# Kernel optimization log

Hardware: AMD Instinct MI355X
Metric: run time of the kernel (lower is better)

Reference implementation:

```python
import jax, jax.numpy as jnp
import numpy as np

B, T, C = 2, 1024, 512
H, KVH = 8, 4
HD = C // H          # head_dim = 64
D2 = HD // 2         # rotary half = 32
SCALE = 1.0 / np.sqrt(HD)


def setup_inputs() -> dict:
    key = jax.random.key(0)
    ks = jax.random.split(key, 5)
    x = jax.random.normal(ks[0], (B, T, C), jnp.float32)
    # RoPE tables: [1, T, 1, D2] broadcastable over (B, T, H, HD/2)
    inv_freq = 1.0 / (10000.0 ** (jnp.arange(D2, dtype=jnp.float32) / D2))
    ang = jnp.arange(T, dtype=jnp.float32)[:, None] * inv_freq[None, :]
    cos = jnp.cos(ang)[None, :, None, :]
    sin = jnp.sin(ang)[None, :, None, :]
    s = 1.0 / np.sqrt(C)
    Wq = jax.random.normal(ks[1], (C, H * HD), jnp.float32) * s
    Wk = jax.random.normal(ks[2], (C, KVH * HD), jnp.float32) * s
    Wv = jax.random.normal(ks[3], (C, KVH * HD), jnp.float32) * s
    Wo = jax.random.normal(ks[4], (C, C), jnp.float32) * s
    return {"x": x, "cos": cos, "sin": sin, "Wq": Wq, "Wk": Wk, "Wv": Wv, "Wo": Wo}


def _rope(t, cos, sin):
    d = t.shape[-1] // 2
    t1, t2 = t[..., :d], t[..., d:]
    return jnp.concatenate([t1 * cos + t2 * sin, -t1 * sin + t2 * cos], axis=-1)


def reference(x, cos, sin, Wq, Wk, Wv, Wo):
    b, t, c = x.shape
    q = (x @ Wq).reshape(b, t, H, HD)
    k = (x @ Wk).reshape(b, t, KVH, HD)
    v = (x @ Wv).reshape(b, t, KVH, HD)
    q = _rope(q, cos, sin)
    k = _rope(k, cos, sin)
    q = q.transpose(0, 2, 1, 3)                      # [B,H,T,HD]
    k = k.transpose(0, 2, 1, 3)                      # [B,KVH,T,HD]
    v = v.transpose(0, 2, 1, 3)
    n_rep = H // KVH
    k = jnp.repeat(k, n_rep, axis=1)                 # GQA expand -> [B,H,T,HD]
    v = jnp.repeat(v, n_rep, axis=1)
    logits = jnp.einsum('bhqd,bhkd->bhqk', q, k) * SCALE
    mask = jnp.triu(jnp.full((t, t), -jnp.inf, dtype=logits.dtype), 1)
    A = jax.nn.softmax(logits + mask, axis=-1)       # [B,H,T,T]
    A_plus_I = A + jnp.eye(t, dtype=A.dtype)
    y = jnp.linalg.solve(A_plus_I, v)                # batched LU solve, (A+I)^-1 @ V
    y = y.transpose(0, 2, 1, 3).reshape(b, t, c)
    return x + y @ Wo
```

## Files before the change

kernel.cpp:

```cpp
#include <hip/hip_runtime.h>
#include <cmath>

#define TT 1024
#define HH 8
#define KVHN 4

typedef unsigned short u16;
typedef __attribute__((ext_vector_type(8))) short bf16x8;
typedef __attribute__((ext_vector_type(4))) float f32x4;

#define MFMA(a, b, c) __builtin_amdgcn_mfma_f32_16x16x32_bf16(a, b, c, 0, 0, 0)

__device__ __forceinline__ float bflo(unsigned u) { return __uint_as_float(u << 16); }
__device__ __forceinline__ float bfhi(unsigned u) { return __uint_as_float(u & 0xffff0000u); }
__device__ __forceinline__ u16 bfr(float f) {
  unsigned u = __float_as_uint(f);
  return (u16)((u + 0x7fffu + ((u >> 16) & 1u)) >> 16);
}
__device__ __forceinline__ float hpart(u16 h) {
  return __uint_as_float((unsigned)h << 16);
}

__device__ __forceinline__ bf16x8 ld8_g(const u16* __restrict__ p) {
  uint4 v = *reinterpret_cast<const uint4*>(p);
  return __builtin_bit_cast(bf16x8, v);
}
__device__ __forceinline__ bf16x8 ld8_lds(const u16* s, int col, int k8) {
  const uint4* p = reinterpret_cast<const uint4*>(s);
  return __builtin_bit_cast(bf16x8, p[col * 8 + (k8 ^ (col & 7))]);
}
__device__ __forceinline__ void st_split_lds(u16* sh, u16* sl, int col, int r0,
                                             f32x4 v) {
  u16 hh[4], ll[4];
#pragma unroll
  for (int j = 0; j < 4; ++j) {
    u16 hb = bfr(v[j]);
    hh[j] = hb;
    ll[j] = bfr(v[j] - hpart(hb));
  }
  uint2 ph, pl;
  ph.x = (unsigned)hh[0] | ((unsigned)hh[1] << 16);
  ph.y = (unsigned)hh[2] | ((unsigned)hh[3] << 16);
  pl.x = (unsigned)ll[0] | ((unsigned)ll[1] << 16);
  pl.y = (unsigned)ll[2] | ((unsigned)ll[3] << 16);
  int idx = col * 64 + (((r0 >> 3) ^ (col & 7)) << 3) + (r0 & 7);
  *reinterpret_cast<uint2*>(sh + idx) = ph;
  *reinterpret_cast<uint2*>(sl + idx) = pl;
}
__device__ __forceinline__ void cvt8v(float4 a, float4 b, bf16x8& h, bf16x8& l) {
  float v[8] = {a.x, a.y, a.z, a.w, b.x, b.y, b.z, b.w};
  unsigned hh[8], ll[8];
#pragma unroll
  for (int j = 0; j < 8; ++j) {
    u16 hb = bfr(v[j]);
    hh[j] = hb;
    ll[j] = bfr(v[j] - hpart(hb));
  }
  uint4 H, L;
  H.x = hh[0] | (hh[1] << 16); H.y = hh[2] | (hh[3] << 16);
  H.z = hh[4] | (hh[5] << 16); H.w = hh[6] | (hh[7] << 16);
  L.x = ll[0] | (ll[1] << 16); L.y = ll[2] | (ll[3] << 16);
  L.z = ll[4] | (ll[5] << 16); L.w = ll[6] | (ll[7] << 16);
  h = __builtin_bit_cast(bf16x8, H);
  l = __builtin_bit_cast(bf16x8, L);
}
__device__ __forceinline__ void cvt8(const float* __restrict__ p, bf16x8& h,
                                     bf16x8& l) {
  float4 a = *reinterpret_cast<const float4*>(p);
  float4 b = *reinterpret_cast<const float4*>(p + 4);
  cvt8v(a, b, h, l);
}

__global__ __launch_bounds__(256) void prep_kernel(
    const float* __restrict__ x, const float* __restrict__ Wq,
    const float* __restrict__ Wk, const float* __restrict__ Wv,
    const float* __restrict__ Wo, u16* __restrict__ WtH, u16* __restrict__ WtL,
    u16* __restrict__ WotH, u16* __restrict__ WotL, u16* __restrict__ Xh,
    u16* __restrict__ Xl) {
  const int kt = blockIdx.x, nt = blockIdx.y;
  const int tid = threadIdx.x;
  const int k0 = kt * 64;

  if (nt >= 24) {
    const int r0 = (nt - 24) * 64;
    const int rr = tid >> 2, kc0 = (tid & 3) * 16;
    const float* src = x + (size_t)(r0 + rr) * 512 + k0 + kc0;
    u16* dh = Xh + (size_t)(r0 + rr) * 512 + k0 + kc0;
    u16* dl = Xl + (size_t)(r0 + rr) * 512 + k0 + kc0;
#pragma unroll
    for (int m = 0; m < 4; ++m) {
      float4 v = *reinterpret_cast<const float4*>(src + m * 4);
      float vv[4] = {v.x, v.y, v.z, v.w};
      u16 hh[4], ll[4];
#pragma unroll
      for (int j = 0; j < 4; ++j) {
        u16 hb = bfr(vv[j]);
        hh[j] = hb;
        ll[j] = bfr(vv[j] - hpart(hb));
      }
      uint2 ph, pl;
      ph.x = (unsigned)hh[0] | ((unsigned)hh[1] << 16);
      ph.y = (unsigned)hh[2] | ((unsigned)hh[3] << 16);
      pl.x = (unsigned)ll[0] | ((unsigned)ll[1] << 16);
      pl.y = (unsigned)ll[2] | ((unsigned)ll[3] << 16);
      *reinterpret_cast<uint2*>(dh + m * 4) = ph;
      *reinterpret_cast<uint2*>(dl + m * 4) = pl;
    }
    return;
  }

  const float* Wsel;
  int wstride, wc0;
  u16 *oh, *ol;
  if (nt < 16) {
    if (nt < 8) { Wsel = Wq; wstride = 512; wc0 = nt * 64; }
    else if (nt < 12) { Wsel = Wk; wstride = 256; wc0 = (nt - 8) * 64; }
    else { Wsel = Wv; wstride = 256; wc0 = (nt - 12) * 64; }
    oh = WtH + (size_t)(nt * 64) * 512;
    ol = WtL + (size_t)(nt * 64) * 512;
  } else {
    Wsel = Wo; wstride = 512; wc0 = (nt - 16) * 64;
    oh = WotH + (size_t)((nt - 16) * 64) * 512;
    ol = WotL + (size_t)((nt - 16) * 64) * 512;
  }

  __shared__ float Ws[64][68];
#pragma unroll
  for (int m = 0; m < 4; ++m) {
    int f = m * 256 + tid;
    int rr = f >> 4, dc = (f & 15) * 4;
    *reinterpret_cast<float4*>(&Ws[rr][dc]) =
        *reinterpret_cast<const float4*>(Wsel + (size_t)(k0 + rr) * wstride + wc0 + dc);
  }
  __syncthreads();

  const int nr = tid >> 2, kc0 = (tid & 3) * 16;
  u16* dh = oh + (size_t)nr * 512 + k0 + kc0;
  u16* dl = ol + (size_t)nr * 512 + k0 + kc0;
#pragma unroll
  for (int i = 0; i < 16; i += 2) {
    float a = Ws[kc0 + i][nr], b = Ws[kc0 + i + 1][nr];
    u16 ha = bfr(a), hb2 = bfr(b);
    u16 la = bfr(a - hpart(ha));
    u16 lb = bfr(b - hpart(hb2));
    *reinterpret_cast<unsigned*>(dh + i) = (unsigned)ha | ((unsigned)hb2 << 16);
    *reinterpret_cast<unsigned*>(dl + i) = (unsigned)la | ((unsigned)lb << 16);
  }
}

__global__ __launch_bounds__(512) void qkv_mfma_kernel(
    const u16* __restrict__ Xh, const u16* __restrict__ Xl,
    const u16* __restrict__ WtH, const u16* __restrict__ WtL,
    const float* __restrict__ cosb, const float* __restrict__ sinb,
    float* __restrict__ Q, float* __restrict__ Kt, float* __restrict__ Vt) {
  const int cy = blockIdx.x, rt = blockIdx.y;
  const int tid = threadIdx.x;
  const int lane = tid & 63, w = tid >> 6;
  const int ln = lane & 15, kg = lane >> 4;
  const int n0 = cy * 64, m0 = rt * 128;

  __shared__ u16 XHs[128 * 64], XLs[128 * 64];
  __shared__ u16 WHs[64 * 64], WLs[64 * 64];

  auto LD8T = [&](const u16* s, int row, int k8) {
    return __builtin_bit_cast(
        bf16x8, reinterpret_cast<const uint4*>(s)[row * 8 + (k8 ^ (row & 7))]);
  };

  f32x4 acc[4];
#pragma unroll
  for (int ct = 0; ct < 4; ++ct) acc[ct] = {0.f, 0.f, 0.f, 0.f};

  for (int c = 0; c < 8; ++c) {
    const int k0 = c * 64;
    __syncthreads();
#pragma unroll
    for (int m = 0; m < 2; ++m) {
      int f = m * 512 + tid;
      int srow = f >> 3, sk8 = f & 7;
      int slot = srow * 8 + (sk8 ^ (srow & 7));
      reinterpret_cast<uint4*>(XHs)[slot] = *reinterpret_cast<const uint4*>(
          Xh + (size_t)(m0 + srow) * 512 + k0 + sk8 * 8);
      reinterpret_cast<uint4*>(XLs)[slot] = *reinterpret_cast<const uint4*>(
          Xl + (size_t)(m0 + srow) * 512 + k0 + sk8 * 8);
    }
    {
      int wrow = tid >> 3, wk8 = tid & 7;
      int slot = wrow * 8 + (wk8 ^ (wrow & 7));
      reinterpret_cast<uint4*>(WHs)[slot] = *reinterpret_cast<const uint4*>(
          WtH + (size_t)(n0 + wrow) * 512 + k0 + wk8 * 8);
      reinterpret_cast<uint4*>(WLs)[slot] = *reinterpret_cast<const uint4*>(
          WtL + (size_t)(n0 + wrow) * 512 + k0 + wk8 * 8);
    }
    __syncthreads();

#pragma unroll
    for (int win = 0; win < 2; ++win) {
      int k8a = win * 4 + kg;
      bf16x8 ah = LD8T(XHs, w * 16 + ln, k8a);
      bf16x8 al = LD8T(XLs, w * 16 + ln, k8a);
#pragma unroll
      for (int ct = 0; ct < 4; ++ct) {
        bf16x8 bh = LD8T(WHs, ct * 16 + ln, k8a);
        bf16x8 bl = LD8T(WLs, ct * 16 + ln, k8a);
        acc[ct] = MFMA(ah, bh, acc[ct]);
        acc[ct] = MFMA(al, bh, acc[ct]);
        acc[ct] = MFMA(ah, bl, acc[ct]);
      }
    }
  }

  const int trow0 = m0 + w * 16 + kg * 4;
  if (cy < 12) {
#pragma unroll
    for (int j = 0; j < 4; ++j) {
      int row = trow0 + j, b = row >> 10, t = row & 1023;
      float* OP;
      size_t base;
      if (cy < 8) {
        OP = Q;
        base = ((size_t)(b * HH + cy) * TT + t) * 64;
      } else {
        OP = Kt;
        base = ((size_t)(b * KVHN + (cy - 8)) * TT + t) * 64;
      }
#pragma unroll
      for (int ct = 0; ct < 2; ++ct) {
        int dd = ct * 16 + ln;
        float cc = cosb[t * 32 + dd], ss = sinb[t * 32 + dd];
        float v1 = acc[ct][j], v2 = acc[ct + 2][j];
        OP[base + dd] = v1 * cc + v2 * ss;
        OP[base + 32 + dd] = v2 * cc - v1 * ss;
      }
    }
  } else {
#pragma unroll
    for (int j = 0; j < 4; ++j) {
      int row = trow0 + j, b = row >> 10, t = row & 1023;
      size_t base = ((size_t)(b * KVHN + (cy - 12)) * TT + t) * 64;
#pragma unroll
      for (int ct = 0; ct < 4; ++ct) Vt[base + ct * 16 + ln] = acc[ct][j];
    }
  }
}

__global__ __launch_bounds__(256) void logits_mfma_kernel(
    const float* __restrict__ Q, const float* __restrict__ Kt,
    u16* __restrict__ A, float* __restrict__ part) {
  const int sys = blockIdx.x, n = blockIdx.y;
  int it = 0;
  while ((it + 1) * (it + 2) / 2 <= n) ++it;
  const int jt = n - it * (it + 1) / 2;
  const int b = sys >> 3, kvh = (sys & 7) >> 1;
  const int tid = threadIdx.x;
  const int lane = tid & 63, w = tid >> 6;
  const int ln = lane & 15, kg = lane >> 4;
  const int m0 = w * 16;

  const float* Qr = Q + ((size_t)sys * TT + it * 64 + m0 + ln) * 64;
  const float* Kb = Kt + ((size_t)(b * KVHN + kvh) * TT + jt * 64) * 64;
  u16* Aout = A + ((size_t)sys << 20);

  bf16x8 qh0, ql0, qh1, ql1;
  cvt8(Qr + kg * 8, qh0, ql0);
  cvt8(Qr + 32 + kg * 8, qh1, ql1);

  f32x4 acc[4];
#pragma unroll
  for (int ct = 0; ct < 4; ++ct) {
    const float* Kr = Kb + (size_t)(ct * 16 + ln) * 64;
    bf16x8 kh0, kl0, kh1, kl1;
    cvt8(Kr + kg * 8, kh0, kl0);
    cvt8(Kr + 32 + kg * 8, kh1, kl1);
    f32x4 a = {0.f, 0.f, 0.f, 0.f};
    a = MFMA(qh0, kh0, a);
    a = MFMA(qh1, kh1, a);
    a = MFMA(qh0, kl0, a);
    a = MFMA(qh1, kl1, a);
    a = MFMA(ql0, kh0, a);
    a = MFMA(ql1, kh1, a);
    acc[ct] = a;
  }

  const int grow0 = it * 64 + m0;
  const bool full = (jt < it);
  float s[4] = {0.f, 0.f, 0.f, 0.f};
#pragma unroll
  for (int ct = 0; ct < 4; ++ct) {
    int col = jt * 64 + ct * 16 + ln;
#pragma unroll
    for (int j = 0; j < 4; ++j) {
      int row = grow0 + kg * 4 + j;
      float e = (full || col <= row) ? __expf(acc[ct][j] * 0.125f) : 0.f;
      s[j] += e;
      Aout[(size_t)row * 1024 + col] = bfr(e);
    }
  }

#pragma unroll
  for (int off = 1; off < 16; off <<= 1) {
#pragma unroll
    for (int j = 0; j < 4; ++j) s[j] += __shfl_xor(s[j], off);
  }
  if (ln == 0) {
#pragma unroll
    for (int j = 0; j < 4; ++j)
      part[((size_t)(sys * 16 + jt)) * 1024 + grow0 + kg * 4 + j] = s[j];
  }
}

__global__ __launch_bounds__(64) void diaginv_kernel(
    u16* __restrict__ A, const float* __restrict__ part,
    float* __restrict__ invs) {
  const int k = blockIdx.x, sys = blockIdx.y;
  const int c = threadIdx.x;

  u16* Ab = A + ((size_t)sys << 20) + (size_t)(k * 64) * 1024 + k * 64;

  __shared__ float MsT[64][68];
  __shared__ float dv[64];

  {
    const int r = c;
    float row[64];
#pragma unroll
    for (int m8 = 0; m8 < 8; ++m8) {
      uint4 v = *reinterpret_cast<const uint4*>(Ab + (size_t)r * 1024 + m8 * 8);
      row[m8 * 8 + 0] = bflo(v.x); row[m8 * 8 + 1] = bfhi(v.x);
      row[m8 * 8 + 2] = bflo(v.y); row[m8 * 8 + 3] = bfhi(v.y);
      row[m8 * 8 + 4] = bflo(v.z); row[m8 * 8 + 5] = bfhi(v.z);
      row[m8 * 8 + 6] = bflo(v.w); row[m8 * 8 + 7] = bfhi(v.w);
    }
    float s = 0.f;
    for (int jt = 0; jt <= k; ++jt)
      s += part[((size_t)(sys * 16 + jt)) * 1024 + k * 64 + r];
    float svr = 1.0f / s;
    invs[sys * 1024 + k * 64 + r] = svr;
    dv[r] = 1.0f / (1.0f + svr * row[r]);
#pragma unroll
    for (int j = 0; j < 64; ++j) MsT[j][r] = svr * row[j];
  }
  __syncthreads();

  float dvr[64];
#pragma unroll
  for (int q = 0; q < 64; ++q) dvr[q] = dv[q];

  float w[64], acc[64];
#pragma unroll
  for (int r = 0; r < 64; ++r) acc[r] = 0.f;

#pragma unroll
  for (int r = 0; r < 64; ++r) {
    float wr = ((r == c) ? 1.0f : 0.0f) - acc[r];
    wr *= dvr[r];
    w[r] = wr;
#pragma unroll
    for (int q = (r + 1) >> 2; q < 16; ++q) {
      float4 m4 = *reinterpret_cast<const float4*>(&MsT[r][q * 4]);
      acc[q * 4 + 0] += m4.x * wr;
      acc[q * 4 + 1] += m4.y * wr;
      acc[q * 4 + 2] += m4.z * wr;
      acc[q * 4 + 3] += m4.w * wr;
    }
  }

#pragma unroll
  for (int r = 0; r < 64; ++r) Ab[(size_t)r * 1024 + c] = bfr(w[r]);
}

__global__ __launch_bounds__(1024) void solve_mfma_kernel(
    const u16* __restrict__ A, const float* __restrict__ invs,
    const float* __restrict__ Vt, float* __restrict__ Yout) {
  const int sys = blockIdx.x, cq = blockIdx.y;
  const int bb = sys >> 3, kvh = (sys & 7) >> 1;
  const int c0 = cq * 16;
  const int tid = threadIdx.x;
  const int lane = tid & 63, w = tid >> 6;
  const int ln = lane & 15, kg = lane >> 4;

  const u16* Ab = A + ((size_t)sys << 20);
  const float* Vb = Vt + ((size_t)(bb * KVHN + kvh) * TT) * 64;
  float* Yg = Yout + (size_t)sys * TT * 64;

  __shared__ float U[16][1031];
  __shared__ u16 yh[16 * 64], yl[16 * 64];
  __shared__ u16 uh[16 * 64], ul[16 * 64];

  {
    float* Uf = &U[0][0];
    for (int i = tid; i < 16 * 1031; i += 1024) Uf[i] = 0.f;
  }
  __syncthreads();

  for (int k = 0; k < 16; ++k) {
    const int rg0 = k * 64;

    uint4 pm0 = {}, pm1 = {};
    f32x4 pv = {0.f, 0.f, 0.f, 0.f}, psi = {0.f, 0.f, 0.f, 0.f};
    if (w < 4) {
      const u16* mrow = Ab + (size_t)(rg0 + w * 16 + ln) * 1024 + rg0;
      pm0 = *reinterpret_cast<const uint4*>(mrow + kg * 8);
      pm1 = *reinterpret_cast<const uint4*>(mrow + 32 + kg * 8);
#pragma unroll
      for (int j = 0; j < 4; ++j) {
        int gr = rg0 + w * 16 + kg * 4 + j;
        pv[j] = Vb[(size_t)gr * 64 + c0 + ln];
        psi[j] = invs[sys * 1024 + gr];
      }
    }
    const int nu = (15 - k) * 4;
    uint4 pa0[4], pa1[4];
    bool val[4];
#pragma unroll
    for (int t = 0; t < 4; ++t) {
      int un = w + 16 * t;
      val[t] = un < nu;
      if (val[t]) {
        const u16* ar =
            Ab + (size_t)((k + 1 + (un >> 2)) * 64 + (un & 3) * 16 + ln) * 1024 +
            rg0;
        pa0[t] = *reinterpret_cast<const uint4*>(ar + kg * 8);
        pa1[t] = *reinterpret_cast<const uint4*>(ar + 32 + kg * 8);
      }
    }
    __builtin_amdgcn_sched_barrier(0);

    if (w < 4) {
      f32x4 u;
#pragma unroll
      for (int j = 0; j < 4; ++j) {
        int gr = rg0 + w * 16 + kg * 4 + j;
        u[j] = pv[j] - psi[j] * U[ln][gr];
      }
      st_split_lds(uh, ul, ln, w * 16 + kg * 4, u);
    }
    __syncthreads();

    if (w < 4) {
      bf16x8 ma0 = __builtin_bit_cast(bf16x8, pm0);
      bf16x8 ma1 = __builtin_bit_cast(bf16x8, pm1);
      f32x4 y = {0.f, 0.f, 0.f, 0.f};
      y = MFMA(ma0, ld8_lds(uh, ln, kg), y);
      y = MFMA(ma1, ld8_lds(uh, ln, 4 + kg), y);
      y = MFMA(ma0, ld8_lds(ul, ln, kg), y);
      y = MFMA(ma1, ld8_lds(ul, ln, 4 + kg), y);
#pragma unroll
      for (int j = 0; j < 4; ++j)
        Yg[(size_t)(rg0 + w * 16 + kg * 4 + j) * 64 + c0 + ln] = y[j];
      st_split_lds(yh, yl, ln, w * 16 + kg * 4, y);
    }
    __syncthreads();

#pragma unroll
    for (int t = 0; t < 4; ++t) {
      if (val[t]) {
        int un = w + 16 * t;
        int rb = (k + 1 + (un >> 2)) * 64 + (un & 3) * 16 + kg * 4;
        bf16x8 a0 = __builtin_bit_cast(bf16x8, pa0[t]);
        bf16x8 a1 = __builtin_bit_cast(bf16x8, pa1[t]);
        f32x4 s = {0.f, 0.f, 0.f, 0.f};
        s = MFMA(a0, ld8_lds(yh, ln, kg), s);
        s = MFMA(a1, ld8_lds(yh, ln, 4 + kg), s);
        s = MFMA(a0, ld8_lds(yl, ln, kg), s);
        s = MFMA(a1, ld8_lds(yl, ln, 4 + kg), s);
#pragma unroll
        for (int j = 0; j < 4; ++j) U[ln][rb + j] += s[j];
      }
    }
    __syncthreads();
  }
}

__global__ __launch_bounds__(256) void out_proj_mfma_kernel(
    const float* __restrict__ Y, const u16* __restrict__ WotH,
    const u16* __restrict__ WotL, const float* __restrict__ x,
    float* __restrict__ out) {
  const int by = blockIdx.x, bx = blockIdx.y;
  const int tid = threadIdx.x;
  const int lane = tid & 63, w = tid >> 6;
  const int wr = w >> 1, wc = w & 1;
  const int ln = lane & 15, kg = lane >> 4;
  const int n0 = by * 64 + wc * 32;
  const int m = bx * 32 + wr * 16 + ln;
  const int b = m >> 10, t = m & 1023;

  const u16* wh0 = WotH + (size_t)(n0 + ln) * 512 + kg * 8;
  const u16* wl0 = WotL + (size_t)(n0 + ln) * 512 + kg * 8;
  const float* Yr = Y + ((size_t)(b * HH) * TT + t) * 64;

  f32x4 acc0 = {0.f, 0.f, 0.f, 0.f}, acc1 = {0.f, 0.f, 0.f, 0.f};

  float4 yA[2], yB[2];
  uint4 fA[4], fB[4];
  auto LD = [&](int kk, float4* yv, uint4* f) {
    const int k0 = kk * 32;
    const int h = k0 >> 6, d0 = (k0 & 63) + kg * 8;
    const float* yp = Yr + (size_t)h * TT * 64 + d0;
    yv[0] = *reinterpret_cast<const float4*>(yp);
    yv[1] = *reinterpret_cast<const float4*>(yp + 4);
    f[0] = *reinterpret_cast<const uint4*>(wh0 + k0);
    f[1] = *reinterpret_cast<const uint4*>(wl0 + k0);
    f[2] = *reinterpret_cast<const uint4*>(wh0 + 16 * 512 + k0);
    f[3] = *reinterpret_cast<const uint4*>(wl0 + 16 * 512 + k0);
  };
  auto FMA = [&](float4* yv, uint4* f) {
    bf16x8 ah, al;
    cvt8v(yv[0], yv[1], ah, al);
    bf16x8 b0h = __builtin_bit_cast(bf16x8, f[0]);
    bf16x8 b0l = __builtin_bit_cast(bf16x8, f[1]);
    bf16x8 b1h = __builtin_bit_cast(bf16x8, f[2]);
    bf16x8 b1l = __builtin_bit_cast(bf16x8, f[3]);
    acc0 = MFMA(ah, b0h, acc0);
    acc0 = MFMA(al, b0h, acc0);
    acc0 = MFMA(ah, b0l, acc0);
    acc1 = MFMA(ah, b1h, acc1);
    acc1 = MFMA(al, b1h, acc1);
    acc1 = MFMA(ah, b1l, acc1);
  };

  LD(0, yA, fA);
#pragma unroll
  for (int k2 = 0; k2 < 8; ++k2) {
    LD(2 * k2 + 1, yB, fB);
    __builtin_amdgcn_sched_barrier(0);
    FMA(yA, fA);
    if (k2 < 7) {
      LD(2 * k2 + 2, yA, fA);
      __builtin_amdgcn_sched_barrier(0);
    }
    FMA(yB, fB);
  }

#pragma unroll
  for (int j = 0; j < 4; ++j) {
    size_t row = (size_t)(bx * 32 + wr * 16 + kg * 4 + j);
    int cc = n0 + ln;
    out[row * 512 + cc] = x[row * 512 + cc] + acc0[j];
    out[row * 512 + cc + 16] = x[row * 512 + cc + 16] + acc1[j];
  }
}

extern "C" void kernel_launch(void* const* d_in, const int* in_sizes, int n_in,
                              void* d_out, int out_size, void* d_ws,
                              size_t ws_size, hipStream_t stream) {
  (void)in_sizes; (void)n_in; (void)out_size; (void)ws_size;
  const float* x = (const float*)d_in[0];
  const float* cosb = (const float*)d_in[1];
  const float* sinb = (const float*)d_in[2];
  const float* Wq = (const float*)d_in[3];
  const float* Wk = (const float*)d_in[4];
  const float* Wv = (const float*)d_in[5];
  const float* Wo = (const float*)d_in[6];
  float* out = (float*)d_out;

  float* ws = (float*)d_ws;
  float* Q = ws;
  float* Kt = Q + (size_t)1048576;
  float* Vt = Kt + (size_t)524288;
  float* Yb = Vt + (size_t)524288;
  float* invs = Yb + (size_t)1048576;
  float* part = invs + (size_t)16384;
  u16* A = (u16*)(part + 262144);
  u16* WtH = A + (size_t)16777216;
  u16* WtL = WtH + (size_t)524288;
  u16* WotH = WtL + (size_t)524288;
  u16* WotL = WotH + (size_t)262144;
  u16* Xh = WotL + (size_t)262144;
  u16* Xl = Xh + (size_t)1048576;

  prep_kernel<<<dim3(8, 56), 256, 0, stream>>>(x, Wq, Wk, Wv, Wo, WtH, WtL,
                                               WotH, WotL, Xh, Xl);
  qkv_mfma_kernel<<<dim3(16, 16), 512, 0, stream>>>(Xh, Xl, WtH, WtL, cosb,
                                                    sinb, Q, Kt, Vt);
  logits_mfma_kernel<<<dim3(16, 136), 256, 0, stream>>>(Q, Kt, A, part);
  diaginv_kernel<<<dim3(16, 16), 64, 0, stream>>>(A, part, invs);
  solve_mfma_kernel<<<dim3(16, 4), 1024, 0, stream>>>(A, invs, Vt, Yb);
  out_proj_mfma_kernel<<<dim3(8, 64), 256, 0, stream>>>(Yb, WotH, WotL, x, out);
}
```

Baseline: 136.9 us.

## Tile output projection through swizzled LDS with 128x64 blocks

Rewrites the output projection kernel so each 512-thread block stages a 128-row Y tile (converted to bf16 hi/lo) and a 64-column Wo tile in XOR-swizzled shared memory. Each wave then computes four 16x16 output tiles from the shared data instead of loading fragments directly from global memory. This cuts redundant global loads and repeated Y conversions across column tiles. In exchange it adds barriers, drops the explicit register double-buffering, and launches fewer blocks (128 instead of 512).

```diff
diff --git a/kernel.cpp b/kernel.cpp
--- a/kernel.cpp
+++ b/kernel.cpp
@@ -472,72 +472,78 @@
   }
 }
 
-__global__ __launch_bounds__(256) void out_proj_mfma_kernel(
+__global__ __launch_bounds__(512) void out_proj_mfma_kernel(
     const float* __restrict__ Y, const u16* __restrict__ WotH,
     const u16* __restrict__ WotL, const float* __restrict__ x,
     float* __restrict__ out) {
-  const int by = blockIdx.x, bx = blockIdx.y;
+  const int cy = blockIdx.x, rt = blockIdx.y;
   const int tid = threadIdx.x;
   const int lane = tid & 63, w = tid >> 6;
-  const int wr = w >> 1, wc = w & 1;
   const int ln = lane & 15, kg = lane >> 4;
-  const int n0 = by * 64 + wc * 32;
-  const int m = bx * 32 + wr * 16 + ln;
-  const int b = m >> 10, t = m & 1023;
-
-  const u16* wh0 = WotH + (size_t)(n0 + ln) * 512 + kg * 8;
-  const u16* wl0 = WotL + (size_t)(n0 + ln) * 512 + kg * 8;
-  const float* Yr = Y + ((size_t)(b * HH) * TT + t) * 64;
-
-  f32x4 acc0 = {0.f, 0.f, 0.f, 0.f}, acc1 = {0.f, 0.f, 0.f, 0.f};
-
-  float4 yA[2], yB[2];
-  uint4 fA[4], fB[4];
-  auto LD = [&](int kk, float4* yv, uint4* f) {
-    const int k0 = kk * 32;
-    const int h = k0 >> 6, d0 = (k0 & 63) + kg * 8;
-    const float* yp = Yr + (size_t)h * TT * 64 + d0;
-    yv[0] = *reinterpret_cast<const float4*>(yp);
-    yv[1] = *reinterpret_cast<const float4*>(yp + 4);
-    f[0] = *reinterpret_cast<const uint4*>(wh0 + k0);
-    f[1] = *reinterpret_cast<const uint4*>(wl0 + k0);
-    f[2] = *reinterpret_cast<const uint4*>(wh0 + 16 * 512 + k0);
-    f[3] = *reinterpret_cast<const uint4*>(wl0 + 16 * 512 + k0);
+  const int n0 = cy * 64, m0 = rt * 128;
+
+  __shared__ u16 YHs[128 * 64], YLs[128 * 64];
+  __shared__ u16 WHs[64 * 64], WLs[64 * 64];
+
+  auto LD8T = [&](const u16* s, int row, int k8) {
+    return __builtin_bit_cast(
+        bf16x8, reinterpret_cast<const uint4*>(s)[row * 8 + (k8 ^ (row & 7))]);
   };
-  auto FMA = [&](float4* yv, uint4* f) {
-    bf16x8 ah, al;
-    cvt8v(yv[0], yv[1], ah, al);
-    bf16x8 b0h = __builtin_bit_cast(bf16x8, f[0]);
-    bf16x8 b0l = __builtin_bit_cast(bf16x8, f[1]);
-    bf16x8 b1h = __builtin_bit_cast(bf16x8, f[2]);
-    bf16x8 b1l = __builtin_bit_cast(bf16x8, f[3]);
-    acc0 = MFMA(ah, b0h, acc0);
-    acc0 = MFMA(al, b0h, acc0);
-    acc0 = MFMA(ah, b0l, acc0);
-    acc1 = MFMA(ah, b1h, acc1);
-    acc1 = MFMA(al, b1h, acc1);
-    acc1 = MFMA(ah, b1l, acc1);
-  };
-
-  LD(0, yA, fA);
-#pragma unroll
-  for (int k2 = 0; k2 < 8; ++k2) {
-    LD(2 * k2 + 1, yB, fB);
-    __builtin_amdgcn_sched_barrier(0);
-    FMA(yA, fA);
-    if (k2 < 7) {
-      LD(2 * k2 + 2, yA, fA);
-      __builtin_amdgcn_sched_barrier(0);
-    }
-    FMA(yB, fB);
-  }
-
+
+  f32x4 acc[4];
+#pragma unroll
+  for (int ct = 0; ct < 4; ++ct) acc[ct] = {0.f, 0.f, 0.f, 0.f};
+
+  for (int c = 0; c < 8; ++c) {
+    const int k0 = c * 64;
+    __syncthreads();
+#pragma unroll
+    for (int m = 0; m < 2; ++m) {
+      int f = m * 512 + tid;
+      int srow = f >> 3, sk8 = f & 7;
+      int slot = srow * 8 + (sk8 ^ (srow & 7));
+      int row = m0 + srow, b = row >> 10, t = row & 1023;
+      const float* yp = Y + ((size_t)(b * HH + c) * TT + t) * 64 + sk8 * 8;
+      bf16x8 h, l;
+      cvt8(yp, h, l);
+      reinterpret_cast<uint4*>(YHs)[slot] = __builtin_bit_cast(uint4, h);
+      reinterpret_cast<uint4*>(YLs)[slot] = __builtin_bit_cast(uint4, l);
+    }
+    {
+      int wrow = tid >> 3, wk8 = tid & 7;
+      int slot = wrow * 8 + (wk8 ^ (wrow & 7));
+      reinterpret_cast<uint4*>(WHs)[slot] = *reinterpret_cast<const uint4*>(
+          WotH + (size_t)(n0 + wrow) * 512 + k0 + wk8 * 8);
+      reinterpret_cast<uint4*>(WLs)[slot] = *reinterpret_cast<const uint4*>(
+          WotL + (size_t)(n0 + wrow) * 512 + k0 + wk8 * 8);
+    }
+    __syncthreads();
+
+#pragma unroll
+    for (int win = 0; win < 2; ++win) {
+      int k8a = win * 4 + kg;
+      bf16x8 ah = LD8T(YHs, w * 16 + ln, k8a);
+      bf16x8 al = LD8T(YLs, w * 16 + ln, k8a);
+#pragma unroll
+      for (int ct = 0; ct < 4; ++ct) {
+        bf16x8 bh = LD8T(WHs, ct * 16 + ln, k8a);
+        bf16x8 bl = LD8T(WLs, ct * 16 + ln, k8a);
+        acc[ct] = MFMA(ah, bh, acc[ct]);
+        acc[ct] = MFMA(al, bh, acc[ct]);
+        acc[ct] = MFMA(ah, bl, acc[ct]);
+      }
+    }
+  }
+
+  const int trow0 = m0 + w * 16 + kg * 4;
 #pragma unroll
   for (int j = 0; j < 4; ++j) {
-    size_t row = (size_t)(bx * 32 + wr * 16 + kg * 4 + j);
-    int cc = n0 + ln;
-    out[row * 512 + cc] = x[row * 512 + cc] + acc0[j];
-    out[row * 512 + cc + 16] = x[row * 512 + cc + 16] + acc1[j];
+    size_t row = (size_t)(trow0 + j);
+#pragma unroll
+    for (int ct = 0; ct < 4; ++ct) {
+      int col = n0 + ct * 16 + ln;
+      out[row * 512 + col] = x[row * 512 + col] + acc[ct][j];
+    }
   }
 }
 
@@ -576,5 +582,5 @@
   logits_mfma_kernel<<<dim3(16, 136), 256, 0, stream>>>(Q, Kt, A, part);
   diaginv_kernel<<<dim3(16, 16), 64, 0, stream>>>(A, part, invs);
   solve_mfma_kernel<<<dim3(16, 4), 1024, 0, stream>>>(A, invs, Vt, Yb);
-  out_proj_mfma_kernel<<<dim3(8, 64), 256, 0, stream>>>(Yb, WotH, WotL, x, out);
-}
+  out_proj_mfma_kernel<<<dim3(8, 16), 512, 0, stream>>>(Yb, WotH, WotL, x, out);
+}
```

Result: faster. 129.8 us, median of 2 (-5.2%).
